# Kernel tuning notes

Hardware: AMD Instinct MI355X
Metric: run time of the kernel (lower is better)

The kernel has to match this reference:

```python
import jax, jax.numpy as jnp
import numpy as np

ALPHA = 0.15  # top-k fraction (forward default)


def setup_inputs() -> dict:
    key = jax.random.key(0)
    k1, k2, k3 = jax.random.split(key, 3)
    B, N, D = 8, 1024, 256
    x = jax.random.normal(k1, (B, N, D), dtype=jnp.float32)
    # torch nn.Linear(dim, H*head_dim, bias=False); stored here as [D, H*head_dim]
    W_src = jax.random.normal(k2, (D, D), dtype=jnp.float32) * (1.0 / np.sqrt(D))
    W_tgt = jax.random.normal(k3, (D, D), dtype=jnp.float32) * (1.0 / np.sqrt(D))
    return {"x": x, "W_src": W_src, "W_tgt": W_tgt}


def _topk_mask(adj, k):
    # adj: [B,H,N,N]; exact scatter of 1.0 at top-k indices along last axis
    B, H, N, _ = adj.shape
    _, idx = jax.lax.top_k(adj, k)              # [B,H,N,k]
    bi = jnp.arange(B)[:, None, None, None]
    hi = jnp.arange(H)[None, :, None, None]
    ni = jnp.arange(N)[None, None, :, None]
    mask = jnp.zeros_like(adj).at[bi, hi, ni, idx].set(1.0)
    return mask


def reference(x, W_src, W_tgt):
    # directed=True path of DirectedGraphLearner.forward
    B, N, D = x.shape
    H, head_dim = 4, D // 4
    k = max(1, int(ALPHA * N))
    src = (x @ W_src).reshape(B, N, H, head_dim)
    tgt = (x @ W_tgt).reshape(B, N, H, head_dim)
    adj = jnp.einsum('bihd,bjhd->bhij', src, tgt)
    adj = jax.nn.gelu(adj, approximate=False)    # torch F.gelu default = exact erf
    mask = _topk_mask(adj, k)
    return adj * mask
```

## Files before the change

kernel.cpp:

```cpp
#include <hip/hip_runtime.h>
#include <math.h>


#define KSEL 153u
#define EPSK 61000u
#define EPSKS 76000u

typedef __attribute__((ext_vector_type(8))) short short8v;
typedef __attribute__((ext_vector_type(4))) float float4v;

__device__ __forceinline__ float gelu_f32(float x) {
    return 0.5f * x * (1.0f + erff(x * 0.70710678118654752f));
}

__device__ __forceinline__ unsigned long long d2key(double v) {
    unsigned long long u = (unsigned long long)__double_as_longlong(v);
    return (u >> 63) ? ~u : (u | 0x8000000000000000ull);
}

__device__ __forceinline__ unsigned lkeyf(float v) {
    float q = fmaf(v, 33554432.0f, 2147483648.0f);
    q = fminf(fmaxf(q, 0.0f), 4294967040.0f);
    return (unsigned)q;
}

__device__ __forceinline__ unsigned short b16(float x) {
    unsigned u = __float_as_uint(x);
    u += 0x7FFFu + ((u >> 16) & 1u);
    return (unsigned short)(u >> 16);
}
__device__ __forceinline__ float bf2f(unsigned short h) {
    return __uint_as_float(((unsigned)h) << 16);
}
__device__ __forceinline__ unsigned pk2(float a, float b) {
    return (unsigned)b16(a) | ((unsigned)b16(b) << 16);
}

#define LGKMW() asm volatile("s_waitcnt lgkmcnt(0)" ::: "memory")
#define LGKM0()                                             \
    do {                                                    \
        asm volatile("s_waitcnt lgkmcnt(0)" ::: "memory");  \
        __builtin_amdgcn_sched_barrier(0);                  \
    } while (0)

template <bool W32>
__global__ __launch_bounds__(256) void k1_proj(const float* __restrict__ x,
                                               const float* __restrict__ Wsrc,
                                               const float* __restrict__ Wtgt,
                                               double* __restrict__ ws,
                                               unsigned short* __restrict__ th,
                                               unsigned short* __restrict__ tl) {
    __shared__ float xs[32 * 68];
    __shared__ float wsh[32 * 68];
    const int t = threadIdx.x;
    const int bx = blockIdx.x;
    const int by = blockIdx.y;
    const int col0 = (by & 3) * 64;
    const float* __restrict__ W = (by < 4) ? Wsrc : Wtgt;
    double* __restrict__ outp = ws + ((by < 4) ? 0 : 2097152);

    double acc[4][4];
#pragma unroll
    for (int i = 0; i < 4; ++i)
#pragma unroll
        for (int j = 0; j < 4; ++j) acc[i][j] = 0.0;

    const int m_loc = (t & 15) * 4;
    const int c_loc = (t >> 4) * 4;

    for (int kt = 0; kt < 8; ++kt) {
        __syncthreads();
#pragma unroll
        for (int it = 0; it < 2; ++it) {
            int f4 = t + 256 * it;
            int m = f4 >> 3, k4 = f4 & 7;
            float4 v = *reinterpret_cast<const float4*>(&x[(bx * 64 + m) * 256 + kt * 32 + 4 * k4]);
            xs[(4 * k4 + 0) * 68 + m] = v.x;
            xs[(4 * k4 + 1) * 68 + m] = v.y;
            xs[(4 * k4 + 2) * 68 + m] = v.z;
            xs[(4 * k4 + 3) * 68 + m] = v.w;
        }
#pragma unroll
        for (int it = 0; it < 2; ++it) {
            int f4 = t + 256 * it;
            int k = f4 >> 4, c4 = f4 & 15;
            *reinterpret_cast<float4*>(&wsh[k * 68 + 4 * c4]) =
                *reinterpret_cast<const float4*>(&W[(kt * 32 + k) * 256 + col0 + 4 * c4]);
        }
        __syncthreads();
#pragma unroll
        for (int kk = 0; kk < 32; ++kk) {
            float4 a = *reinterpret_cast<const float4*>(&xs[kk * 68 + m_loc]);
            float4 b = *reinterpret_cast<const float4*>(&wsh[kk * 68 + c_loc]);
            double ad[4] = {a.x, a.y, a.z, a.w};
            double bd[4] = {b.x, b.y, b.z, b.w};
#pragma unroll
            for (int i = 0; i < 4; ++i)
#pragma unroll
                for (int j = 0; j < 4; ++j) acc[i][j] += ad[i] * bd[j];
        }
    }
    const int hd = by & 3;
#pragma unroll
    for (int i = 0; i < 4; ++i) {
        int m = bx * 64 + m_loc + i;
        int b = m >> 10, n = m & 1023;
        int bhd = b * 4 + hd;
        size_t base = ((size_t)(bhd * 1024 + n)) * 64 + c_loc;
        double2 v01, v23;
        v01.x = acc[i][0]; v01.y = acc[i][1];
        v23.x = acc[i][2]; v23.y = acc[i][3];
        *reinterpret_cast<double2*>(&outp[base]) = v01;
        *reinterpret_cast<double2*>(&outp[base + 2]) = v23;
        if (W32 && by >= 4) {
            float f0 = (float)acc[i][0], f1 = (float)acc[i][1];
            float f2 = (float)acc[i][2], f3 = (float)acc[i][3];
            unsigned short h0 = b16(f0), h1 = b16(f1), h2 = b16(f2), h3 = b16(f3);
            uint2 H, L;
            H.x = (unsigned)h0 | ((unsigned)h1 << 16);
            H.y = (unsigned)h2 | ((unsigned)h3 << 16);
            L.x = pk2(f0 - bf2f(h0), f1 - bf2f(h1));
            L.y = pk2(f2 - bf2f(h2), f3 - bf2f(h3));
            int T = n >> 4, colLow = n & 15;
            int ks = c_loc >> 5, kg = (c_loc >> 3) & 3, elem = c_loc & 7;
            size_t fidx = ((size_t)bhd * 65536) +
                          (size_t)(((T * 2 + ks) * 64 + kg * 16 + colLow) * 8 + elem);
            *reinterpret_cast<uint2*>(&th[fidx]) = H;
            *reinterpret_cast<uint2*>(&tl[fidx]) = L;
        }
    }
}

template <bool FAST, bool S16, bool SIDE>
__global__ __launch_bounds__(256, SIDE ? 3 : 4) void k2a_gemm(
    const double* __restrict__ srcT, const double* __restrict__ tgtT,
    const unsigned short* __restrict__ th, const unsigned short* __restrict__ tlo,
    short* __restrict__ adjS, unsigned short* __restrict__ side,
    float* __restrict__ out) {
    __shared__ __align__(16) float tr[16 * 512];
    __shared__ __align__(16) unsigned rhist[SIDE ? 4 * 4 * 256 : 4];

    unsigned short* sHI = reinterpret_cast<unsigned short*>(tr);
    unsigned short* sLO = sHI + 1024;

    const int t = threadIdx.x;
    const int lane = t & 63;
    const int wv = t >> 6;
    const int bid = (blockIdx.x & 7) * 256 + (blockIdx.x >> 3);
    const int bh = bid >> 6;
    const int itile = bid & 63;
    const int row0 = itile * 16;
    const int r0 = 4 * wv;
    const size_t tgtBase = (size_t)bh * 65536;
    const unsigned short* __restrict__ thb = th + tgtBase;
    const unsigned short* __restrict__ tlb = tlo + tgtBase;

    if (SIDE) {
#pragma unroll
        for (int e = 0; e < 4; ++e)
            *reinterpret_cast<uint4*>(&rhist[4 * t + 1024 * e]) = make_uint4(0u, 0u, 0u, 0u);
    }
    {
        int r = t >> 4, dq = (t & 15) * 4;
        const double* sp = &srcT[((size_t)bh * 1024 + row0 + r) * 64 + dq];
        double2 a = *reinterpret_cast<const double2*>(sp);
        double2 b = *reinterpret_cast<const double2*>(sp + 2);
        float f0 = (float)a.x, f1 = (float)a.y, f2 = (float)b.x, f3 = (float)b.y;
        unsigned short h0 = b16(f0), h1 = b16(f1), h2 = b16(f2), h3 = b16(f3);
        int s = dq >> 3;
        int idx = r * 64 + ((s ^ (r & 7)) << 3) + (dq & 7);
        uint2 H, L;
        H.x = (unsigned)h0 | ((unsigned)h1 << 16);
        H.y = (unsigned)h2 | ((unsigned)h3 << 16);
        L.x = pk2(f0 - bf2f(h0), f1 - bf2f(h1));
        L.y = pk2(f2 - bf2f(h2), f3 - bf2f(h3));
        *reinterpret_cast<uint2*>(&sHI[idx]) = H;
        *reinterpret_cast<uint2*>(&sLO[idx]) = L;
    }
    __syncthreads();

    short8v Ah[2], Al[2];
#pragma unroll
    for (int ks = 0; ks < 2; ++ks) {
        int idxA = (lane & 15) * 64 + (((4 * ks + (lane >> 4)) ^ (lane & 7)) << 3);
        Ah[ks] = *reinterpret_cast<const short8v*>(&sHI[idxA]);
        Al[ks] = *reinterpret_cast<const short8v*>(&sLO[idxA]);
    }

    const int colA = lane & 15;
    const int kgrp = lane >> 4;
    const size_t rowG0 = (size_t)bh * 1024 + row0 + r0;

#pragma unroll
    for (int h = 0; h < 2; ++h) {
        float4v acc[8];
#pragma unroll
        for (int a = 0; a < 8; ++a) acc[a] = (float4v){0.f, 0.f, 0.f, 0.f};

#pragma unroll
        for (int u = 0; u < 8; ++u) {
            const int T = 32 * h + 4 * u + wv;
#pragma unroll
            for (int ks = 0; ks < 2; ++ks) {
                short8v Bh, Bl;
                if (FAST) {
                    const size_t fbase = (size_t)(((T * 2 + ks) * 64 + lane) * 8);
                    Bh = *reinterpret_cast<const short8v*>(&thb[fbase]);
                    Bl = *reinterpret_cast<const short8v*>(&tlb[fbase]);
                } else {
                    const size_t cbase = (size_t)(16 * T + colA) * 64 + kgrp * 8;
                    const double* gp = &tgtT[tgtBase + cbase + 32 * ks];
                    double2 d0 = *reinterpret_cast<const double2*>(gp);
                    double2 d1 = *reinterpret_cast<const double2*>(gp + 2);
                    double2 d2 = *reinterpret_cast<const double2*>(gp + 4);
                    double2 d3 = *reinterpret_cast<const double2*>(gp + 6);
                    float f[8] = {(float)d0.x, (float)d0.y, (float)d1.x, (float)d1.y,
                                  (float)d2.x, (float)d2.y, (float)d3.x, (float)d3.y};
                    unsigned short hh[8];
#pragma unroll
                    for (int e = 0; e < 8; ++e) hh[e] = b16(f[e]);
                    unsigned Hw[4], Lw[4];
#pragma unroll
                    for (int e = 0; e < 4; ++e) {
                        Hw[e] = (unsigned)hh[2 * e] | ((unsigned)hh[2 * e + 1] << 16);
                        Lw[e] = pk2(f[2 * e] - bf2f(hh[2 * e]), f[2 * e + 1] - bf2f(hh[2 * e + 1]));
                    }
                    Bh = *reinterpret_cast<const short8v*>(Hw);
                    Bl = *reinterpret_cast<const short8v*>(Lw);
                }
                acc[u] = __builtin_amdgcn_mfma_f32_16x16x32_bf16(Ah[ks], Bh, acc[u], 0, 0, 0);
                acc[u] = __builtin_amdgcn_mfma_f32_16x16x32_bf16(Al[ks], Bh, acc[u], 0, 0, 0);
                acc[u] = __builtin_amdgcn_mfma_f32_16x16x32_bf16(Ah[ks], Bl, acc[u], 0, 0, 0);
            }
        }

        __syncthreads();
#pragma unroll
        for (int u = 0; u < 8; ++u) {
            int colh = 16 * (4 * u + wv) + colA;
#pragma unroll
            for (int reg = 0; reg < 4; ++reg) {
                int row = 4 * kgrp + reg;
                tr[row * 512 + (colh ^ ((kgrp & 1) << 4))] = acc[u][reg];
            }
        }
        __syncthreads();
        const int rsw = (wv & 1) << 4;
#pragma unroll
        for (int ri = 0; ri < 4; ++ri) {
            int row = r0 + ri;
#pragma unroll
            for (int q = 0; q < 2; ++q) {
                int colh = 4 * lane + 256 * q;
                float4 v = *reinterpret_cast<const float4*>(&tr[row * 512 + (colh ^ rsw)]);
                float vv[4] = {v.x, v.y, v.z, v.w};
                if (S16) {
                    short ss[4];
#pragma unroll
                    for (int e = 0; e < 4; ++e)
                        ss[e] = (short)__float2int_rn(fminf(fmaxf(vv[e] * 512.f, -32767.f), 32767.f));
                    short4 s;
                    s.x = ss[0]; s.y = ss[1]; s.z = ss[2]; s.w = ss[3];
                    *reinterpret_cast<short4*>(&adjS[(rowG0 + ri) * 1024 + 512 * h + colh]) = s;
                    if (SIDE) {
#pragma unroll
                        for (int e = 0; e < 4; ++e) {
                            float vd = (float)ss[e] * (1.0f / 512.0f);
                            atomicAdd(&rhist[(4 * wv + ri) * 256 + (lkeyf(vd) >> 24)], 1u);
                        }
                    }
                } else {
                    *reinterpret_cast<float4*>(&out[(rowG0 + ri) * 1024 + 512 * h + colh]) = v;
                    if (SIDE) {
#pragma unroll
                        for (int e = 0; e < 4; ++e)
                            atomicAdd(&rhist[(4 * wv + ri) * 256 + (lkeyf(vv[e]) >> 24)], 1u);
                    }
                }
            }
        }
    }

    if (SIDE) {
        LGKMW();
#pragma unroll 1
        for (int ri = 0; ri < 4; ++ri) {
            uint4 hv = *reinterpret_cast<const uint4*>(&rhist[(4 * wv + ri) * 256 + 4 * lane]);
            unsigned h0 = hv.x, h1 = hv.y, h2 = hv.z, h3 = hv.w;
            unsigned S = h0 + h1 + h2 + h3;
            unsigned inc = S;
#pragma unroll
            for (int off = 1; off < 64; off <<= 1) {
                unsigned o = __shfl_down(inc, off, 64);
                inc = (lane + off < 64) ? (inc + o) : inc;
            }
            unsigned above = inc - S;
            unsigned rk = KSEL;
            bool found = (above < rk) && (rk <= inc);
            unsigned long long bal = __ballot(found);
            int L = __ffsll(bal) - 1;
            unsigned hh[4];
            hh[0] = __shfl(h0, L, 64);
            hh[1] = __shfl(h1, L, 64);
            hh[2] = __shfl(h2, L, 64);
            hh[3] = __shfl(h3, L, 64);
            unsigned cum = __shfl(above, L, 64);
            int bsel = -1;
#pragma unroll
            for (int q = 3; q >= 0; --q) {
                if (bsel < 0) {
                    if (rk <= cum + hh[q]) {
                        bsel = q;
                        rk = rk - cum;
                    } else {
                        cum += hh[q];
                    }
                }
            }
            if (lane == 0)
                side[rowG0 + ri] = (unsigned short)(((unsigned)(4 * L + bsel) << 8) | rk);
        }
    }
}

template <bool S16, bool SIDE>
__global__ __launch_bounds__(256, 4) void k2b_select(const double* __restrict__ srcT,
                                                     const double* __restrict__ tgtT,
                                                     const short* __restrict__ adjS,
                                                     const unsigned short* __restrict__ side,
                                                     float* __restrict__ out) {
    __shared__ __align__(16) unsigned hist[4][256];

    const int t = threadIdx.x;
    const int lane = t & 63;
    const int wv = t >> 6;
    const int R = blockIdx.x * 4 + wv;
    const int bh = R >> 10;
    const size_t tgtBase = (size_t)bh * 65536;
    const size_t base = (size_t)R * 1024;
    const unsigned eps = S16 ? EPSKS : EPSK;

    float vals[16];
    if (S16) {
#pragma unroll
        for (int q = 0; q < 2; ++q) {
            short8v s = *reinterpret_cast<const short8v*>(&adjS[base + 16 * lane + 8 * q]);
#pragma unroll
            for (int e = 0; e < 8; ++e) vals[8 * q + e] = (float)s[e] * (1.0f / 512.0f);
        }
    } else {
#pragma unroll
        for (int q = 0; q < 4; ++q) {
            float4 v = *reinterpret_cast<const float4*>(&out[base + 16 * lane + 4 * q]);
            vals[4 * q + 0] = v.x;
            vals[4 * q + 1] = v.y;
            vals[4 * q + 2] = v.z;
            vals[4 * q + 3] = v.w;
        }
    }

    unsigned* histw = hist[wv];
    unsigned* cjp = histw + 128;
    unsigned long long* ckp = reinterpret_cast<unsigned long long*>(histw);
    unsigned* ccp = histw + 192;

    unsigned ul[16];
#pragma unroll
    for (int m = 0; m < 16; ++m) ul[m] = lkeyf(vals[m]);

    unsigned prefA, maskA, rk;
    if (SIDE) {
        unsigned sd = side[R];
        prefA = (sd >> 8) << 24;
        maskA = 0xFF000000u;
        rk = sd & 255u;
    } else {
        prefA = 0u; maskA = 0u; rk = KSEL;
    }

#pragma unroll 1
    for (int p = (SIDE ? 0 : 1); p >= 0; --p) {
        const int sh = 16 + 8 * p;
        *reinterpret_cast<uint4*>(&histw[4 * lane]) = make_uint4(0u, 0u, 0u, 0u);
        LGKMW();
#pragma unroll
        for (int m = 0; m < 16; ++m) {
            if ((ul[m] & maskA) == prefA)
                atomicAdd(&histw[(ul[m] >> sh) & 255u], 1u);
        }
        LGKMW();
        unsigned h0 = histw[4 * lane + 0], h1 = histw[4 * lane + 1];
        unsigned h2 = histw[4 * lane + 2], h3 = histw[4 * lane + 3];
        unsigned S = h0 + h1 + h2 + h3;
        unsigned inc = S;
#pragma unroll
        for (int off = 1; off < 64; off <<= 1) {
            unsigned o = __shfl_down(inc, off, 64);
            inc = (lane + off < 64) ? (inc + o) : inc;
        }
        unsigned above = inc - S;
        bool found = (above < rk) && (rk <= inc);
        unsigned long long bal = __ballot(found);
        int L = __ffsll(bal) - 1;
        unsigned hh[4];
        hh[0] = __shfl(h0, L, 64);
        hh[1] = __shfl(h1, L, 64);
        hh[2] = __shfl(h2, L, 64);
        hh[3] = __shfl(h3, L, 64);
        unsigned cum = __shfl(above, L, 64);
        int bsel = -1;
#pragma unroll
        for (int q = 3; q >= 0; --q) {
            if (bsel < 0) {
                if (rk <= cum + hh[q]) {
                    bsel = q;
                    rk = rk - cum;
                } else {
                    cum += hh[q];
                }
            }
        }
        prefA |= (unsigned)(4 * L + bsel) << sh;
        maskA |= 0xFFu << sh;
    }

    const unsigned klo = prefA - eps;
    const unsigned khi = prefA + 65535u + eps;

    int ch = 0, cb = 0;
#pragma unroll
    for (int m = 0; m < 16; ++m) {
        ch += (ul[m] > khi) ? 1 : 0;
        cb += (ul[m] >= klo && ul[m] <= khi) ? 1 : 0;
    }
#pragma unroll
    for (int off = 32; off; off >>= 1) {
        ch += __shfl_xor(ch, off, 64);
        cb += __shfl_xor(cb, off, 64);
    }
    const unsigned need = KSEL - (unsigned)ch;
    const bool fastp = ((unsigned)cb == need);

    unsigned long long selMask = 0ull;
    unsigned cidx[16];
    if (!fastp) {
        if (lane == 0) *ccp = 0u;
        LGKM0();
#pragma unroll
        for (int m = 0; m < 16; ++m) {
            cidx[m] = 0xFFFFFFFFu;
            if (ul[m] >= klo && ul[m] <= khi) {
                unsigned idx = atomicAdd(ccp, 1u);
                cidx[m] = idx;
                if (idx < 64u) cjp[idx] = (unsigned)(16 * lane + m);
            }
        }
        LGKM0();
        unsigned g = *ccp;
        if (g > 64u) g = 64u;
        if (lane < (int)g) {
            unsigned j = cjp[lane];
            const double2* sp = reinterpret_cast<const double2*>(&srcT[(size_t)R * 64]);
            const double2* tp = reinterpret_cast<const double2*>(&tgtT[tgtBase + (size_t)j * 64]);
            double a2 = 0.0;
#pragma unroll 8
            for (int d2 = 0; d2 < 32; ++d2) {
                double2 aa = sp[d2], bb = tp[d2];
                a2 = fma(aa.x, bb.x, fma(aa.y, bb.y, a2));
            }
            ckp[lane] = d2key(a2);
        }
        LGKM0();
        unsigned rnk2 = need;
        if (lane < (int)g) {
            unsigned long long myk = ckp[lane];
            unsigned myj = cjp[lane];
            rnk2 = 0;
            for (unsigned i = 0; i < g; ++i) {
                unsigned long long ki = ckp[i];
                rnk2 += (ki > myk || (ki == myk && cjp[i] < myj)) ? 1u : 0u;
            }
        }
        selMask = __ballot(lane < (int)g && rnk2 < need);
    }

#pragma unroll
    for (int q = 0; q < 4; ++q) {
        float4 o;
        float* op = &o.x;
#pragma unroll
        for (int e = 0; e < 4; ++e) {
            int m = 4 * q + e;
            bool sel;
            if (ul[m] > khi) sel = true;
            else if (ul[m] < klo) sel = false;
            else sel = fastp ? true
                             : ((cidx[m] < 64u) ? (((selMask >> cidx[m]) & 1ull) != 0ull) : false);
            float v = vals[m];
            op[e] = sel ? ((v > 3.0f) ? v : gelu_f32(v)) : 0.0f;
        }
        *reinterpret_cast<float4*>(&out[base + 16 * lane + 4 * q]) = o;
    }
}

extern "C" void kernel_launch(void* const* d_in, const int* in_sizes, int n_in,
                              void* d_out, int out_size, void* d_ws, size_t ws_size,
                              hipStream_t stream) {
    const float* x = (const float*)d_in[0];
    const float* Wsrc = (const float*)d_in[1];
    const float* Wtgt = (const float*)d_in[2];
    float* out = (float*)d_out;
    double* ws = (double*)d_ws;
    unsigned short* th = (unsigned short*)((char*)d_ws + 33554432);
    unsigned short* tl = (unsigned short*)((char*)d_ws + 37748736);
    short* adjS = (short*)((char*)d_ws + 41943040);
    unsigned short* side = (unsigned short*)((char*)d_ws + 109051904);

    const bool fast = (ws_size >= 40u * 1024u * 1024u);
    const bool s16 = (ws_size >= 104u * 1024u * 1024u);
    const bool sideok = (ws_size >= 110u * 1024u * 1024u);
    dim3 g1(128, 8);
    if (fast && s16 && sideok) {
        k1_proj<true><<<g1, 256, 0, stream>>>(x, Wsrc, Wtgt, ws, th, tl);
        k2a_gemm<true, true, true><<<2048, 256, 0, stream>>>(ws, ws + 2097152, th, tl, adjS, side, out);
        k2b_select<true, true><<<8192, 256, 0, stream>>>(ws, ws + 2097152, adjS, side, out);
    } else if (fast && s16) {
        k1_proj<true><<<g1, 256, 0, stream>>>(x, Wsrc, Wtgt, ws, th, tl);
        k2a_gemm<true, true, false><<<2048, 256, 0, stream>>>(ws, ws + 2097152, th, tl, adjS, side, out);
        k2b_select<true, false><<<8192, 256, 0, stream>>>(ws, ws + 2097152, adjS, side, out);
    } else if (fast) {
        k1_proj<true><<<g1, 256, 0, stream>>>(x, Wsrc, Wtgt, ws, th, tl);
        k2a_gemm<true, false, false><<<2048, 256, 0, stream>>>(ws, ws + 2097152, th, tl, adjS, side, out);
        k2b_select<false, false><<<8192, 256, 0, stream>>>(ws, ws + 2097152, adjS, side, out);
    } else {
        k1_proj<false><<<g1, 256, 0, stream>>>(x, Wsrc, Wtgt, ws, th, tl);
        k2a_gemm<false, false, false><<<2048, 256, 0, stream>>>(ws, ws + 2097152, th, tl, adjS, side, out);
        k2b_select<false, false><<<8192, 256, 0, stream>>>(ws, ws + 2097152, adjS, side, out);
    }
}
```

Baseline: 165.1 us.

## Fuse top-k selection into the GEMM kernel, dropping the separate select launch

The top-k selection (second radix histogram pass, candidate refinement with exact double dot products, GELU and masked output write) moves into the tail of the GEMM kernel. Each wave reads back its own 16-bit rows from adjS right after writing them. This removes the third kernel launch, the side-channel buffer and the re-read of adjS by a separate grid. In exchange the GEMM blocks carry more work and registers at 3 blocks per CU, and the selection runs with only 2048 blocks instead of 8192, which cuts parallelism for that phase.

```diff
diff --git a/kernel.cpp b/kernel.cpp
--- a/kernel.cpp
+++ b/kernel.cpp
@@ -131,14 +131,13 @@
     }
 }
 
-template <bool FAST, bool S16, bool SIDE>
-__global__ __launch_bounds__(256, SIDE ? 3 : 4) void k2a_gemm(
+template <bool FAST, bool FUSE>
+__global__ __launch_bounds__(256, FUSE ? 3 : 4) void k2a_gemm(
     const double* __restrict__ srcT, const double* __restrict__ tgtT,
     const unsigned short* __restrict__ th, const unsigned short* __restrict__ tlo,
-    short* __restrict__ adjS, unsigned short* __restrict__ side,
-    float* __restrict__ out) {
+    short* __restrict__ adjS, float* __restrict__ out) {
     __shared__ __align__(16) float tr[16 * 512];
-    __shared__ __align__(16) unsigned rhist[SIDE ? 4 * 4 * 256 : 4];
+    __shared__ __align__(16) unsigned rhist[FUSE ? 4 * 4 * 256 : 4];
 
     unsigned short* sHI = reinterpret_cast<unsigned short*>(tr);
     unsigned short* sLO = sHI + 1024;
@@ -155,7 +154,7 @@
     const unsigned short* __restrict__ thb = th + tgtBase;
     const unsigned short* __restrict__ tlb = tlo + tgtBase;
 
-    if (SIDE) {
+    if (FUSE) {
 #pragma unroll
         for (int e = 0; e < 4; ++e)
             *reinterpret_cast<uint4*>(&rhist[4 * t + 1024 * e]) = make_uint4(0u, 0u, 0u, 0u);
@@ -254,7 +253,7 @@
                 int colh = 4 * lane + 256 * q;
                 float4 v = *reinterpret_cast<const float4*>(&tr[row * 512 + (colh ^ rsw)]);
                 float vv[4] = {v.x, v.y, v.z, v.w};
-                if (S16) {
+                if (FUSE) {
                     short ss[4];
 #pragma unroll
                     for (int e = 0; e < 4; ++e)
@@ -262,72 +261,203 @@
                     short4 s;
                     s.x = ss[0]; s.y = ss[1]; s.z = ss[2]; s.w = ss[3];
                     *reinterpret_cast<short4*>(&adjS[(rowG0 + ri) * 1024 + 512 * h + colh]) = s;
-                    if (SIDE) {
-#pragma unroll
-                        for (int e = 0; e < 4; ++e) {
-                            float vd = (float)ss[e] * (1.0f / 512.0f);
-                            atomicAdd(&rhist[(4 * wv + ri) * 256 + (lkeyf(vd) >> 24)], 1u);
-                        }
+#pragma unroll
+                    for (int e = 0; e < 4; ++e) {
+                        float vd = (float)ss[e] * (1.0f / 512.0f);
+                        atomicAdd(&rhist[(4 * wv + ri) * 256 + (lkeyf(vd) >> 24)], 1u);
                     }
                 } else {
                     *reinterpret_cast<float4*>(&out[(rowG0 + ri) * 1024 + 512 * h + colh]) = v;
-                    if (SIDE) {
-#pragma unroll
-                        for (int e = 0; e < 4; ++e)
-                            atomicAdd(&rhist[(4 * wv + ri) * 256 + (lkeyf(vv[e]) >> 24)], 1u);
-                    }
-                }
-            }
-        }
-    }
-
-    if (SIDE) {
-        LGKMW();
+                }
+            }
+        }
+    }
+
+    if (FUSE) {
+        asm volatile("s_waitcnt vmcnt(0) lgkmcnt(0)" ::: "memory");
 #pragma unroll 1
         for (int ri = 0; ri < 4; ++ri) {
-            uint4 hv = *reinterpret_cast<const uint4*>(&rhist[(4 * wv + ri) * 256 + 4 * lane]);
-            unsigned h0 = hv.x, h1 = hv.y, h2 = hv.z, h3 = hv.w;
-            unsigned S = h0 + h1 + h2 + h3;
-            unsigned inc = S;
-#pragma unroll
-            for (int off = 1; off < 64; off <<= 1) {
-                unsigned o = __shfl_down(inc, off, 64);
-                inc = (lane + off < 64) ? (inc + o) : inc;
-            }
-            unsigned above = inc - S;
-            unsigned rk = KSEL;
-            bool found = (above < rk) && (rk <= inc);
-            unsigned long long bal = __ballot(found);
-            int L = __ffsll(bal) - 1;
-            unsigned hh[4];
-            hh[0] = __shfl(h0, L, 64);
-            hh[1] = __shfl(h1, L, 64);
-            hh[2] = __shfl(h2, L, 64);
-            hh[3] = __shfl(h3, L, 64);
-            unsigned cum = __shfl(above, L, 64);
-            int bsel = -1;
-#pragma unroll
-            for (int q = 3; q >= 0; --q) {
-                if (bsel < 0) {
-                    if (rk <= cum + hh[q]) {
-                        bsel = q;
-                        rk = rk - cum;
-                    } else {
-                        cum += hh[q];
+            const size_t rowR = rowG0 + ri;
+            unsigned* hw = &rhist[(4 * wv + ri) * 256];
+            unsigned* cjp = hw + 128;
+            unsigned long long* ckp = reinterpret_cast<unsigned long long*>(hw);
+            unsigned* ccp = hw + 192;
+
+            float vals[16];
+#pragma unroll
+            for (int q = 0; q < 2; ++q) {
+                short8v s = *reinterpret_cast<const short8v*>(&adjS[rowR * 1024 + 16 * lane + 8 * q]);
+#pragma unroll
+                for (int e = 0; e < 8; ++e) vals[8 * q + e] = (float)s[e] * (1.0f / 512.0f);
+            }
+            unsigned ul[16];
+#pragma unroll
+            for (int m = 0; m < 16; ++m) ul[m] = lkeyf(vals[m]);
+
+            unsigned prefA = 0u, rk = KSEL;
+            {
+                uint4 hv = *reinterpret_cast<const uint4*>(&hw[4 * lane]);
+                unsigned h0 = hv.x, h1 = hv.y, h2 = hv.z, h3 = hv.w;
+                unsigned S = h0 + h1 + h2 + h3;
+                unsigned inc = S;
+#pragma unroll
+                for (int off = 1; off < 64; off <<= 1) {
+                    unsigned o = __shfl_down(inc, off, 64);
+                    inc = (lane + off < 64) ? (inc + o) : inc;
+                }
+                unsigned above = inc - S;
+                bool found = (above < rk) && (rk <= inc);
+                unsigned long long bal = __ballot(found);
+                int L = __ffsll(bal) - 1;
+                unsigned hh[4];
+                hh[0] = __shfl(h0, L, 64);
+                hh[1] = __shfl(h1, L, 64);
+                hh[2] = __shfl(h2, L, 64);
+                hh[3] = __shfl(h3, L, 64);
+                unsigned cum = __shfl(above, L, 64);
+                int bsel = -1;
+#pragma unroll
+                for (int q = 3; q >= 0; --q) {
+                    if (bsel < 0) {
+                        if (rk <= cum + hh[q]) {
+                            bsel = q;
+                            rk = rk - cum;
+                        } else {
+                            cum += hh[q];
+                        }
                     }
                 }
-            }
-            if (lane == 0)
-                side[rowG0 + ri] = (unsigned short)(((unsigned)(4 * L + bsel) << 8) | rk);
-        }
-    }
-}
-
-template <bool S16, bool SIDE>
+                prefA = (unsigned)(4 * L + bsel) << 24;
+            }
+
+            *reinterpret_cast<uint4*>(&hw[4 * lane]) = make_uint4(0u, 0u, 0u, 0u);
+            LGKMW();
+#pragma unroll
+            for (int m = 0; m < 16; ++m) {
+                if ((ul[m] & 0xFF000000u) == prefA)
+                    atomicAdd(&hw[(ul[m] >> 16) & 255u], 1u);
+            }
+            LGKMW();
+            {
+                unsigned h0 = hw[4 * lane + 0], h1 = hw[4 * lane + 1];
+                unsigned h2 = hw[4 * lane + 2], h3 = hw[4 * lane + 3];
+                unsigned S = h0 + h1 + h2 + h3;
+                unsigned inc = S;
+#pragma unroll
+                for (int off = 1; off < 64; off <<= 1) {
+                    unsigned o = __shfl_down(inc, off, 64);
+                    inc = (lane + off < 64) ? (inc + o) : inc;
+                }
+                unsigned above = inc - S;
+                bool found = (above < rk) && (rk <= inc);
+                unsigned long long bal = __ballot(found);
+                int L = __ffsll(bal) - 1;
+                unsigned hh[4];
+                hh[0] = __shfl(h0, L, 64);
+                hh[1] = __shfl(h1, L, 64);
+                hh[2] = __shfl(h2, L, 64);
+                hh[3] = __shfl(h3, L, 64);
+                unsigned cum = __shfl(above, L, 64);
+                int bsel = -1;
+#pragma unroll
+                for (int q = 3; q >= 0; --q) {
+                    if (bsel < 0) {
+                        if (rk <= cum + hh[q]) {
+                            bsel = q;
+                            rk = rk - cum;
+                        } else {
+                            cum += hh[q];
+                        }
+                    }
+                }
+                prefA |= (unsigned)(4 * L + bsel) << 16;
+            }
+
+            const unsigned klo = prefA - EPSKS;
+            const unsigned khi = prefA + 65535u + EPSKS;
+
+            int ch = 0, cb = 0;
+#pragma unroll
+            for (int m = 0; m < 16; ++m) {
+                ch += (ul[m] > khi) ? 1 : 0;
+                cb += (ul[m] >= klo && ul[m] <= khi) ? 1 : 0;
+            }
+#pragma unroll
+            for (int off = 32; off; off >>= 1) {
+                ch += __shfl_xor(ch, off, 64);
+                cb += __shfl_xor(cb, off, 64);
+            }
+            const unsigned need = KSEL - (unsigned)ch;
+            const bool fastp = ((unsigned)cb == need);
+
+            unsigned long long selMask = 0ull;
+            unsigned cidx[16];
+            if (!fastp) {
+                if (lane == 0) *ccp = 0u;
+                LGKM0();
+#pragma unroll
+                for (int m = 0; m < 16; ++m) {
+                    cidx[m] = 0xFFFFFFFFu;
+                    if (ul[m] >= klo && ul[m] <= khi) {
+                        unsigned idx = atomicAdd(ccp, 1u);
+                        cidx[m] = idx;
+                        if (idx < 64u) cjp[idx] = (unsigned)(16 * lane + m);
+                    }
+                }
+                LGKM0();
+                unsigned g = *ccp;
+                if (g > 64u) g = 64u;
+                if (lane < (int)g) {
+                    unsigned j = cjp[lane];
+                    const double2* sp = reinterpret_cast<const double2*>(&srcT[rowR * 64]);
+                    const double2* tp =
+                        reinterpret_cast<const double2*>(&tgtT[tgtBase + (size_t)j * 64]);
+                    double a2 = 0.0;
+#pragma unroll 8
+                    for (int d2 = 0; d2 < 32; ++d2) {
+                        double2 aa = sp[d2], bb = tp[d2];
+                        a2 = fma(aa.x, bb.x, fma(aa.y, bb.y, a2));
+                    }
+                    ckp[lane] = d2key(a2);
+                }
+                LGKM0();
+                unsigned rnk2 = need;
+                if (lane < (int)g) {
+                    unsigned long long myk = ckp[lane];
+                    unsigned myj = cjp[lane];
+                    rnk2 = 0;
+                    for (unsigned i = 0; i < g; ++i) {
+                        unsigned long long ki = ckp[i];
+                        rnk2 += (ki > myk || (ki == myk && cjp[i] < myj)) ? 1u : 0u;
+                    }
+                }
+                selMask = __ballot(lane < (int)g && rnk2 < need);
+            }
+
+#pragma unroll
+            for (int q = 0; q < 4; ++q) {
+                float4 o;
+                float* op = &o.x;
+#pragma unroll
+                for (int e = 0; e < 4; ++e) {
+                    int m = 4 * q + e;
+                    bool sel;
+                    if (ul[m] > khi) sel = true;
+                    else if (ul[m] < klo) sel = false;
+                    else sel = fastp ? true
+                                     : ((cidx[m] < 64u) ? (((selMask >> cidx[m]) & 1ull) != 0ull)
+                                                        : false);
+                    float v = vals[m];
+                    op[e] = sel ? ((v > 3.0f) ? v : gelu_f32(v)) : 0.0f;
+                }
+                *reinterpret_cast<float4*>(&out[rowR * 1024 + 16 * lane + 4 * q]) = o;
+            }
+        }
+    }
+}
+
 __global__ __launch_bounds__(256, 4) void k2b_select(const double* __restrict__ srcT,
                                                      const double* __restrict__ tgtT,
-                                                     const short* __restrict__ adjS,
-                                                     const unsigned short* __restrict__ side,
                                                      float* __restrict__ out) {
     __shared__ __align__(16) unsigned hist[4][256];
 
@@ -338,25 +468,15 @@
     const int bh = R >> 10;
     const size_t tgtBase = (size_t)bh * 65536;
     const size_t base = (size_t)R * 1024;
-    const unsigned eps = S16 ? EPSKS : EPSK;
 
     float vals[16];
-    if (S16) {
-#pragma unroll
-        for (int q = 0; q < 2; ++q) {
-            short8v s = *reinterpret_cast<const short8v*>(&adjS[base + 16 * lane + 8 * q]);
-#pragma unroll
-            for (int e = 0; e < 8; ++e) vals[8 * q + e] = (float)s[e] * (1.0f / 512.0f);
-        }
-    } else {
-#pragma unroll
-        for (int q = 0; q < 4; ++q) {
-            float4 v = *reinterpret_cast<const float4*>(&out[base + 16 * lane + 4 * q]);
-            vals[4 * q + 0] = v.x;
-            vals[4 * q + 1] = v.y;
-            vals[4 * q + 2] = v.z;
-            vals[4 * q + 3] = v.w;
-        }
+#pragma unroll
+    for (int q = 0; q < 4; ++q) {
+        float4 v = *reinterpret_cast<const float4*>(&out[base + 16 * lane + 4 * q]);
+        vals[4 * q + 0] = v.x;
+        vals[4 * q + 1] = v.y;
+        vals[4 * q + 2] = v.z;
+        vals[4 * q + 3] = v.w;
     }
 
     unsigned* histw = hist[wv];
@@ -368,18 +488,9 @@
 #pragma unroll
     for (int m = 0; m < 16; ++m) ul[m] = lkeyf(vals[m]);
 
-    unsigned prefA, maskA, rk;
-    if (SIDE) {
-        unsigned sd = side[R];
-        prefA = (sd >> 8) << 24;
-        maskA = 0xFF000000u;
-        rk = sd & 255u;
-    } else {
-        prefA = 0u; maskA = 0u; rk = KSEL;
-    }
-
+    unsigned prefA = 0u, maskA = 0u, rk = KSEL;
 #pragma unroll 1
-    for (int p = (SIDE ? 0 : 1); p >= 0; --p) {
+    for (int p = 1; p >= 0; --p) {
         const int sh = 16 + 8 * p;
         *reinterpret_cast<uint4*>(&histw[4 * lane]) = make_uint4(0u, 0u, 0u, 0u);
         LGKMW();
@@ -424,8 +535,8 @@
         maskA |= 0xFFu << sh;
     }
 
-    const unsigned klo = prefA - eps;
-    const unsigned khi = prefA + 65535u + eps;
+    const unsigned klo = prefA - EPSK;
+    const unsigned khi = prefA + 65535u + EPSK;
 
     int ch = 0, cb = 0;
 #pragma unroll
@@ -514,27 +625,20 @@
     unsigned short* th = (unsigned short*)((char*)d_ws + 33554432);
     unsigned short* tl = (unsigned short*)((char*)d_ws + 37748736);
     short* adjS = (short*)((char*)d_ws + 41943040);
-    unsigned short* side = (unsigned short*)((char*)d_ws + 109051904);
 
     const bool fast = (ws_size >= 40u * 1024u * 1024u);
-    const bool s16 = (ws_size >= 104u * 1024u * 1024u);
-    const bool sideok = (ws_size >= 110u * 1024u * 1024u);
+    const bool fuse = (ws_size >= 104u * 1024u * 1024u);
     dim3 g1(128, 8);
-    if (fast && s16 && sideok) {
+    if (fast && fuse) {
         k1_proj<true><<<g1, 256, 0, stream>>>(x, Wsrc, Wtgt, ws, th, tl);
-        k2a_gemm<true, true, true><<<2048, 256, 0, stream>>>(ws, ws + 2097152, th, tl, adjS, side, out);
-        k2b_select<true, true><<<8192, 256, 0, stream>>>(ws, ws + 2097152, adjS, side, out);
-    } else if (fast && s16) {
-        k1_proj<true><<<g1, 256, 0, stream>>>(x, Wsrc, Wtgt, ws, th, tl);
-        k2a_gemm<true, true, false><<<2048, 256, 0, stream>>>(ws, ws + 2097152, th, tl, adjS, side, out);
-        k2b_select<true, false><<<8192, 256, 0, stream>>>(ws, ws + 2097152, adjS, side, out);
+        k2a_gemm<true, true><<<2048, 256, 0, stream>>>(ws, ws + 2097152, th, tl, adjS, out);
     } else if (fast) {
         k1_proj<true><<<g1, 256, 0, stream>>>(x, Wsrc, Wtgt, ws, th, tl);
-        k2a_gemm<true, false, false><<<2048, 256, 0, stream>>>(ws, ws + 2097152, th, tl, adjS, side, out);
-        k2b_select<false, false><<<8192, 256, 0, stream>>>(ws, ws + 2097152, adjS, side, out);
+        k2a_gemm<true, false><<<2048, 256, 0, stream>>>(ws, ws + 2097152, th, tl, adjS, out);
+        k2b_select<<<8192, 256, 0, stream>>>(ws, ws + 2097152, out);
     } else {
         k1_proj<false><<<g1, 256, 0, stream>>>(x, Wsrc, Wtgt, ws, th, tl);
-        k2a_gemm<false, false, false><<<2048, 256, 0, stream>>>(ws, ws + 2097152, th, tl, adjS, side, out);
-        k2b_select<false, false><<<8192, 256, 0, stream>>>(ws, ws + 2097152, adjS, side, out);
-    }
-}
+        k2a_gemm<false, false><<<2048, 256, 0, stream>>>(ws, ws + 2097152, th, tl, adjS, out);
+        k2b_select<<<8192, 256, 0, stream>>>(ws, ws + 2097152, out);
+    }
+}
```

Measured after the change: 163.3 us. About the same (-1.1%).
